# Performance work log

Hardware: AMD Instinct MI355X
Metric: run time of the kernel (lower is better)

Reference implementation:

```python
import jax, jax.numpy as jnp
import numpy as np

NB_KNN = 10
T = 0.07
NUM_CLASSES = 50
EPS = 1e-12  # torch F.normalize eps


def _l2norm(x, axis):
    n = jnp.sqrt(jnp.sum(x * x, axis=axis, keepdims=True))
    return x / jnp.maximum(n, EPS)


def setup_inputs() -> dict:
    key = jax.random.key(0)
    k1, k2, k3 = jax.random.split(key, 3)
    B, N, D = 1024, 200000, 256
    test_features = jax.random.normal(k1, (B, D), dtype=jnp.float32)
    train_features = jax.random.normal(k2, (N, D), dtype=jnp.float32)
    train_labels = jax.random.randint(k3, (N,), 0, NUM_CLASSES, dtype=jnp.int64)
    return {
        "test_features": test_features,
        "train_features": train_features,
        "train_labels": train_labels,
    }


def reference(test_features, train_features, train_labels):
    # Faithful to torch: normalize(train_features.T, dim=1) -> normalize [D, N]
    # along axis 1 (the N axis), exactly as the original module does.
    gallery = _l2norm(train_features.T, axis=1)          # [D, N]
    q = _l2norm(test_features, axis=1)                   # [B, D]
    sim = q @ gallery                                    # [B, N]
    topk_sims, idx = jax.lax.top_k(sim, NB_KNN)          # [B, k], [B, k]
    neighbors_labels = train_labels[idx]                 # [B, k]
    w = jax.nn.softmax(topk_sims / T, axis=1)            # [B, k]
    # one-hot weighted scatter-sum into class scores
    onehot = jax.nn.one_hot(neighbors_labels, NUM_CLASSES, dtype=w.dtype)  # [B, k, C]
    return jnp.sum(onehot * w[:, :, None], axis=1)       # [B, C]
```

## Files before the change

### kernel.cpp

```cpp
#include <hip/hip_runtime.h>
#include <hip/hip_bf16.h>
#include <math.h>
#include <stdint.h>

#define DDIM 256
#define CAP  320
#define NCLS 50

typedef short bf16x8_t __attribute__((ext_vector_type(8)));
typedef float f32x4_t  __attribute__((ext_vector_type(4)));

__device__ __forceinline__ void gl_lds16(const void* g, void* l) {
  __builtin_amdgcn_global_load_lds(
      (__attribute__((address_space(1))) unsigned int*)(uintptr_t)g,
      (__attribute__((address_space(3))) unsigned int*)l,
      16, 0, 0);
}

__global__ void k_cast_colsq(const float* __restrict__ train,
                             __hip_bfloat16* __restrict__ tbf,
                             double* __restrict__ colsq, int N) {
  const int t = threadIdx.x;
  const int nb = gridDim.x;
  const int per = (N + nb - 1) / nb;
  const int r0 = blockIdx.x * per;
  const int r1 = (r0 + per < N) ? (r0 + per) : N;
  double acc = 0.0;
  int r = r0;
  for (; r + 4 <= r1; r += 4) {
    float v0 = train[(size_t)(r + 0) * DDIM + t];
    float v1 = train[(size_t)(r + 1) * DDIM + t];
    float v2 = train[(size_t)(r + 2) * DDIM + t];
    float v3 = train[(size_t)(r + 3) * DDIM + t];
    if (tbf) {
      tbf[(size_t)(r + 0) * DDIM + t] = __float2bfloat16(v0);
      tbf[(size_t)(r + 1) * DDIM + t] = __float2bfloat16(v1);
      tbf[(size_t)(r + 2) * DDIM + t] = __float2bfloat16(v2);
      tbf[(size_t)(r + 3) * DDIM + t] = __float2bfloat16(v3);
    }
    acc = fma((double)v0, (double)v0, acc);
    acc = fma((double)v1, (double)v1, acc);
    acc = fma((double)v2, (double)v2, acc);
    acc = fma((double)v3, (double)v3, acc);
  }
  for (; r < r1; ++r) {
    float v = train[(size_t)r * DDIM + t];
    if (tbf) tbf[(size_t)r * DDIM + t] = __float2bfloat16(v);
    acc = fma((double)v, (double)v, acc);
  }
  atomicAdd(&colsq[t], acc);
}

__global__ void k_prep(const float* __restrict__ test, const double* __restrict__ colsq,
                       float* __restrict__ qs, __hip_bfloat16* __restrict__ qs_bf,
                       float* __restrict__ tau, int B) {
  const int row = blockIdx.x, t = threadIdx.x;
  const int wid = t >> 6, lane = t & 63;
  __shared__ float ps[4];
  __shared__ float stot;
  float v = test[(size_t)row * DDIM + t];
  float ss = v * v;
#pragma unroll
  for (int o = 32; o > 0; o >>= 1) ss += __shfl_down(ss, o, 64);
  if (lane == 0) ps[wid] = ss;
  __syncthreads();
  if (t == 0) stot = ps[0] + ps[1] + ps[2] + ps[3];
  __syncthreads();
  float rn   = fmaxf(sqrtf(stot), 1e-12f);
  float coln = fmaxf(sqrtf((float)colsq[t]), 1e-12f);
  float qv   = (v / rn) / coln;
  qs[(size_t)row * DDIM + t] = qv;
  qs_bf[(size_t)row * DDIM + t] = __float2bfloat16(qv);
  float s2 = qv * qv;
#pragma unroll
  for (int o = 32; o > 0; o >>= 1) s2 += __shfl_down(s2, o, 64);
  if (lane == 0) ps[wid] = s2;
  __syncthreads();
  if (t == 0) tau[row] = 3.30f * sqrtf(ps[0] + ps[1] + ps[2] + ps[3]);
}

__global__ __launch_bounds__(256, 3)
void k_mfma(const __hip_bfloat16* __restrict__ qs_bf,
            const __hip_bfloat16* __restrict__ train_bf,
            const float* __restrict__ tau, int* __restrict__ cidx,
            int* __restrict__ cnt, int N, int B) {
  __shared__ __align__(16) char sAB[2][16384];
  __shared__ float tau_s[128];
  const int tid = threadIdx.x;
  const int w = tid >> 6, lane = tid & 63;
  const int wr = w >> 1, wc = w & 1;
  const int row0 = blockIdx.y * 128;
  const int col0 = blockIdx.x * 128;
  const int l15 = lane & 15, l4 = lane >> 4;

  if (tid < 128) {
    int rr = row0 + tid; if (rr >= B) rr = B - 1;
    tau_s[tid] = tau[rr];
  }

  const int g0 = 2 * w, g1 = 2 * w + 1;
  int ar0 = row0 + g0 * 16 + l15; if (ar0 >= B) ar0 = B - 1;
  int ar1 = row0 + g1 * 16 + l15; if (ar1 >= B) ar1 = B - 1;
  const __hip_bfloat16* aS0 = qs_bf + (size_t)ar0 * DDIM + l4 * 8;
  const __hip_bfloat16* aS1 = qs_bf + (size_t)ar1 * DDIM + l4 * 8;
  int bc0 = col0 + g0 * 16 + l15; if (bc0 >= N) bc0 = N - 1;
  int bc1 = col0 + g1 * 16 + l15; if (bc1 >= N) bc1 = N - 1;
  const __hip_bfloat16* bS0 = train_bf + (size_t)bc0 * DDIM + l4 * 8;
  const __hip_bfloat16* bS1 = train_bf + (size_t)bc1 * DDIM + l4 * 8;

  f32x4_t acc[4][4];
#pragma unroll
  for (int m = 0; m < 4; ++m)
#pragma unroll
    for (int n = 0; n < 4; ++n) acc[m][n] = (f32x4_t){0.f, 0.f, 0.f, 0.f};

  {
    char* A0 = sAB[0]; char* B0 = sAB[0] + 8192;
    gl_lds16(aS0, A0 + g0 * 1024);
    gl_lds16(aS1, A0 + g1 * 1024);
    gl_lds16(bS0, B0 + g0 * 1024);
    gl_lds16(bS1, B0 + g1 * 1024);
  }
  __syncthreads();

  for (int s = 0; s < 8; ++s) {
    const int cur = s & 1;
    if (s < 7) {
      const int ko = (s + 1) * 32;
      char* An = sAB[cur ^ 1]; char* Bn = An + 8192;
      gl_lds16(aS0 + ko, An + g0 * 1024);
      gl_lds16(aS1 + ko, An + g1 * 1024);
      gl_lds16(bS0 + ko, Bn + g0 * 1024);
      gl_lds16(bS1 + ko, Bn + g1 * 1024);
    }
    const char* Ac = sAB[cur]; const char* Bc = Ac + 8192;
    bf16x8_t af[4], bfr[4];
#pragma unroll
    for (int m = 0; m < 4; ++m)
      af[m] = *(const bf16x8_t*)(Ac + (wr * 4 + m) * 1024 + lane * 16);
#pragma unroll
    for (int n = 0; n < 4; ++n)
      bfr[n] = *(const bf16x8_t*)(Bc + (wc * 4 + n) * 1024 + lane * 16);
#pragma unroll
    for (int m = 0; m < 4; ++m)
#pragma unroll
      for (int n = 0; n < 4; ++n)
        acc[m][n] = __builtin_amdgcn_mfma_f32_16x16x32_bf16(af[m], bfr[n],
                                                            acc[m][n], 0, 0, 0);
    __syncthreads();
  }

#pragma unroll
  for (int m = 0; m < 4; ++m) {
#pragma unroll
    for (int n = 0; n < 4; ++n) {
      const int col = col0 + wc * 64 + n * 16 + l15;
      if (col < N) {
#pragma unroll
        for (int r = 0; r < 4; ++r) {
          const int rl = wr * 64 + m * 16 + l4 * 4 + r;
          if (acc[m][n][r] > tau_s[rl] && row0 + rl < B) {
            int p = atomicAdd(&cnt[row0 + rl], 1);
            if (p < CAP) cidx[(size_t)(row0 + rl) * CAP + p] = col;
          }
        }
      }
    }
  }
}

#define DOT4(ACC, A, Bv)                                                     \
  ACC = fmaf((A).x, (Bv).x, ACC); ACC = fmaf((A).y, (Bv).y, ACC);            \
  ACC = fmaf((A).z, (Bv).z, ACC); ACC = fmaf((A).w, (Bv).w, ACC);

__global__ __launch_bounds__(256, 4)
void k_gemm(const float* __restrict__ train, const float* __restrict__ qs,
            const float* __restrict__ tau, int* __restrict__ cidx,
            int* __restrict__ cnt, int N, int B, int tpc) {
  __shared__ float4 As4[8 * 128];
  __shared__ float4 Bs4[8 * 64];
  const int tid = threadIdx.x;
  const int tx = tid & 15, ty = tid >> 4;
  const int wid = tid >> 6, lane = tid & 63;
  const int row0 = blockIdx.y * 128;
  const int colbase = blockIdx.x * tpc * 64;
  float tau_r[8];
#pragma unroll
  for (int i = 0; i < 8; ++i) {
    int r = row0 + ty + 16 * i; if (r >= B) r = B - 1;
    tau_r[i] = tau[r];
  }
  int rL = row0 + lane;      if (rL >= B) rL = B - 1;
  int rH = row0 + 64 + lane; if (rH >= B) rH = B - 1;
  const float* aptrL = qs + (size_t)rL * DDIM;
  const float* aptrH = qs + (size_t)rH * DDIM;
  for (int tile = 0; tile < tpc; ++tile) {
    const int col0 = colbase + tile * 64;
    if (col0 >= N) break;
    int bcol = col0 + lane; if (bcol >= N) bcol = N - 1;
    const float* bptr = train + (size_t)bcol * DDIM;
    float acc[8][4];
#pragma unroll
    for (int i = 0; i < 8; ++i)
#pragma unroll
      for (int j = 0; j < 4; ++j) acc[i][j] = 0.f;
    for (int s = 0; s < 8; ++s) {
      const int kk0 = s * 32;
      __syncthreads();
#pragma unroll
      for (int j = 0; j < 4; ++j) {
        const int slot = wid + 4 * j;
        const int m = slot >> 1, half = slot & 1;
        gl_lds16((half ? aptrH : aptrL) + kk0 + 4 * m, &As4[m * 128 + half * 64]);
      }
#pragma unroll
      for (int j = 0; j < 2; ++j) {
        const int m = wid + 4 * j;
        gl_lds16(bptr + kk0 + 4 * m, &Bs4[m * 64]);
      }
      __syncthreads();
#pragma unroll
      for (int k4 = 0; k4 < 8; ++k4) {
        float4 a[8], b[4];
#pragma unroll
        for (int i = 0; i < 8; ++i) a[i] = As4[k4 * 128 + ty + 16 * i];
#pragma unroll
        for (int j = 0; j < 4; ++j) b[j] = Bs4[k4 * 64 + tx + 16 * j];
#pragma unroll
        for (int i = 0; i < 8; ++i)
#pragma unroll
          for (int j = 0; j < 4; ++j) { DOT4(acc[i][j], a[i], b[j]) }
      }
    }
#pragma unroll
    for (int i = 0; i < 8; ++i) {
      const int r = row0 + ty + 16 * i;
#pragma unroll
      for (int j = 0; j < 4; ++j) {
        const int c = col0 + tx + 16 * j;
        if (acc[i][j] > tau_r[i] && c < N && r < B) {
          int p = atomicAdd(&cnt[r], 1);
          if (p < CAP) cidx[(size_t)r * CAP + p] = c;
        }
      }
    }
  }
}

__global__ void k_fallback(const float* __restrict__ train, const float* __restrict__ qs,
                           int* __restrict__ cidx, int* __restrict__ cnt, int N) {
  const int row = blockIdx.x;
  const int t = threadIdx.x;
  const int c0 = cnt[row];
  if (c0 >= 10 && c0 <= CAP) return;
  __shared__ float q[DDIM];
  if (t < DDIM) q[t] = qs[(size_t)row * DDIM + t];
  __syncthreads();
  float lv[10]; int li[10];
#pragma unroll
  for (int k = 0; k < 10; ++k) { lv[k] = -INFINITY; li[k] = 0x7FFFFFFF; }
  for (int c = t; c < N; c += 256) {
    const float* tr = train + (size_t)c * DDIM;
    float s = 0.f;
    for (int d = 0; d < DDIM; ++d) s = fmaf(q[d], tr[d], s);
    if (s > lv[9]) {
      int p = 9;
      while (p > 0 && s > lv[p - 1]) { lv[p] = lv[p - 1]; li[p] = li[p - 1]; --p; }
      lv[p] = s; li[p] = c;
    }
  }
  __shared__ float rv[256]; __shared__ int ri[256]; __shared__ int rt_[256];
  __shared__ int topi[10];
  int pt = 0;
  for (int k = 0; k < 10; ++k) {
    rv[t] = (pt < 10) ? lv[pt] : -INFINITY;
    ri[t] = (pt < 10) ? li[pt] : 0x7FFFFFFF;
    rt_[t] = t;
    __syncthreads();
    for (int s2 = 128; s2 > 0; s2 >>= 1) {
      if (t < s2) {
        float ov = rv[t + s2]; int oi = ri[t + s2];
        if (ov > rv[t] || (ov == rv[t] && oi < ri[t])) {
          rv[t] = ov; ri[t] = oi; rt_[t] = rt_[t + s2];
        }
      }
      __syncthreads();
    }
    const int win = rt_[0];
    if (t == 0) topi[k] = ri[0];
    __syncthreads();
    if (t == win) ++pt;
  }
  if (t < 10) cidx[(size_t)row * CAP + t] = topi[t];
  if (t == 0) cnt[row] = 10;
}

__global__ void k_rescore(const float* __restrict__ train, const float* __restrict__ qs,
                          const int* __restrict__ cidx, const int* __restrict__ cnt,
                          double* __restrict__ dval) {
  const int row = blockIdx.x;
  const int t = threadIdx.x, wid = t >> 6, lane = t & 63;
  __shared__ float qsh[DDIM];
  if (t < DDIM) qsh[t] = qs[(size_t)row * DDIM + t];
  __syncthreads();
  int n = cnt[row]; if (n > CAP) n = CAP;
  for (int ci = wid; ci < n; ci += 4) {
    const int c = cidx[(size_t)row * CAP + ci];
    const float4 tv = *(const float4*)(train + (size_t)c * DDIM + lane * 4);
    const float4 qv = *(const float4*)(qsh + lane * 4);
    double s = (double)tv.x * qv.x + (double)tv.y * qv.y +
               (double)tv.z * qv.z + (double)tv.w * qv.w;
#pragma unroll
    for (int o = 32; o > 0; o >>= 1) s += __shfl_down(s, o, 64);
    if (lane == 0) dval[(size_t)row * CAP + ci] = s;
  }
}

__global__ void k_finalize(const double* __restrict__ dval, const int* __restrict__ cidx,
                           const int* __restrict__ cnt, const int* __restrict__ labels,
                           float* __restrict__ out) {
  const int row = blockIdx.x;
  const int t = threadIdx.x;
  int n = cnt[row]; if (n > CAP) n = CAP;
  __shared__ double sv[CAP]; __shared__ int si[CAP];
  for (int i = t; i < CAP; i += 256) {
    sv[i] = (i < n) ? dval[(size_t)row * CAP + i] : -INFINITY;
    si[i] = (i < n) ? cidx[(size_t)row * CAP + i] : 0x7FFFFFFF;
  }
  __syncthreads();
  __shared__ double rv[256]; __shared__ int ri[256]; __shared__ int rp[256];
  __shared__ double topv[10]; __shared__ int topl[10];
  __shared__ int wpos;
  for (int k = 0; k < 10; ++k) {
    double bv = sv[t]; int bi = si[t]; int bp = t;
    if (t + 256 < CAP) {
      double v2 = sv[t + 256]; int i2 = si[t + 256];
      if (v2 > bv || (v2 == bv && i2 < bi)) { bv = v2; bi = i2; bp = t + 256; }
    }
    rv[t] = bv; ri[t] = bi; rp[t] = bp;
    __syncthreads();
    for (int s2 = 128; s2 > 0; s2 >>= 1) {
      if (t < s2) {
        double ov = rv[t + s2]; int oi = ri[t + s2];
        if (ov > rv[t] || (ov == rv[t] && oi < ri[t])) {
          rv[t] = ov; ri[t] = oi; rp[t] = rp[t + s2];
        }
      }
      __syncthreads();
    }
    if (t == 0) { topv[k] = rv[0]; topl[k] = ri[0]; wpos = rp[0]; }
    __syncthreads();
    if (t == 0) sv[wpos] = -INFINITY;
    __syncthreads();
  }
  __shared__ double oc[NCLS];
  if (t < NCLS) oc[t] = 0.0;
  __syncthreads();
  if (t == 0) {
    const double m = topv[0];
    double w[10]; double ssum = 0.0;
#pragma unroll
    for (int k = 0; k < 10; ++k) { w[k] = exp((topv[k] - m) / 0.07); ssum += w[k]; }
#pragma unroll
    for (int k = 0; k < 10; ++k) oc[labels[topl[k]]] += w[k] / ssum;
  }
  __syncthreads();
  if (t < NCLS) out[(size_t)row * NCLS + t] = (float)oc[t];
}

extern "C" void kernel_launch(void* const* d_in, const int* in_sizes, int n_in,
                              void* d_out, int out_size, void* d_ws, size_t ws_size,
                              hipStream_t stream) {
  const float* test   = (const float*)d_in[0];
  const float* train  = (const float*)d_in[1];
  const int*   labels = (const int*)d_in[2];
  float* out = (float*)d_out;
  const int B = in_sizes[0] / DDIM;
  const int N = in_sizes[2];
  (void)n_in; (void)out_size;

  char* w = (char*)d_ws;
  size_t off = 0;
  auto alloc = [&](size_t bytes) {
    size_t o = off; off = (off + bytes + 255) & ~(size_t)255; return o;
  };
  double* colsq = (double*)(w + alloc(2048));
  int*    cnt   = (int*)(w + alloc((size_t)B * 4));
  float*  tau   = (float*)(w + alloc((size_t)B * 4));
  float*  qs    = (float*)(w + alloc((size_t)B * DDIM * 4));
  __hip_bfloat16* qs_bf = (__hip_bfloat16*)(w + alloc((size_t)B * DDIM * 2));
  int*    cidx  = (int*)(w + alloc((size_t)B * CAP * 4));
  double* dval  = (double*)(w + alloc((size_t)B * CAP * 8));
  __hip_bfloat16* train_bf = (__hip_bfloat16*)(w + alloc((size_t)N * DDIM * 2));
  const bool use_mfma = (ws_size >= off);

  hipMemsetAsync(d_ws, 0, 2048 + (size_t)B * 4, stream);

  if (use_mfma) {
    hipLaunchKernelGGL(k_cast_colsq, dim3(1024), dim3(256), 0, stream,
                       train, train_bf, colsq, N);
    hipLaunchKernelGGL(k_prep, dim3(B), dim3(256), 0, stream,
                       test, colsq, qs, qs_bf, tau, B);
    hipLaunchKernelGGL(k_mfma, dim3((N + 127) / 128, (B + 127) / 128),
                       dim3(256), 0, stream, qs_bf, train_bf, tau, cidx, cnt, N, B);
  } else {
    hipLaunchKernelGGL(k_cast_colsq, dim3(1024), dim3(256), 0, stream,
                       train, (__hip_bfloat16*)nullptr, colsq, N);
    hipLaunchKernelGGL(k_prep, dim3(B), dim3(256), 0, stream,
                       test, colsq, qs, qs_bf, tau, B);
    const int CT = (N + 63) / 64;
    const int rb = (B + 127) / 128;
    int bx = 2048 / (rb > 0 ? rb : 1); if (bx < 1) bx = 1;
    int tpc = (CT + bx - 1) / bx;
    int chunks = (CT + tpc - 1) / tpc;
    hipLaunchKernelGGL(k_gemm, dim3(chunks, rb), dim3(256), 0, stream,
                       train, qs, tau, cidx, cnt, N, B, tpc);
  }

  hipLaunchKernelGGL(k_fallback, dim3(B), dim3(256), 0, stream,
                     train, qs, cidx, cnt, N);
  hipLaunchKernelGGL(k_rescore,  dim3(B), dim3(256), 0, stream,
                     train, qs, cidx, cnt, dval);
  hipLaunchKernelGGL(k_finalize, dim3(B), dim3(256), 0, stream,
                     dval, cidx, cnt, labels, out);
}
```

Baseline: 619.1 us.

## Keep train tile resident in LDS and stream all query panels per block

The MFMA similarity kernel now loads a full 128-column train tile (all 256 dims, 64KB) into LDS once, then loops over every 128-row query panel. A fragments are read directly from global memory and prefetched one K-step ahead, so the train matrix is read once instead of once per query panel. The cast/column-norm kernel is also vectorized to float4 loads with ushort4 bf16 stores and an LDS reduction, and its grid is halved. The trade-offs are lower occupancy from the 64KB LDS footprint and A operands coming from global/L2 rather than shared memory.

```diff
diff --git a/kernel.cpp b/kernel.cpp
--- a/kernel.cpp
+++ b/kernel.cpp
@@ -17,38 +17,41 @@
       16, 0, 0);
 }
 
+__device__ __forceinline__ unsigned short bf16bits(float v) {
+  __hip_bfloat16 h = __float2bfloat16(v);
+  return *reinterpret_cast<unsigned short*>(&h);
+}
+
 __global__ void k_cast_colsq(const float* __restrict__ train,
                              __hip_bfloat16* __restrict__ tbf,
                              double* __restrict__ colsq, int N) {
   const int t = threadIdx.x;
+  const int rsub = t >> 6;
+  const int c4 = (t & 63) * 4;
   const int nb = gridDim.x;
-  const int per = (N + nb - 1) / nb;
+  int per = (N + nb - 1) / nb; per = (per + 3) & ~3;
   const int r0 = blockIdx.x * per;
-  const int r1 = (r0 + per < N) ? (r0 + per) : N;
-  double acc = 0.0;
-  int r = r0;
-  for (; r + 4 <= r1; r += 4) {
-    float v0 = train[(size_t)(r + 0) * DDIM + t];
-    float v1 = train[(size_t)(r + 1) * DDIM + t];
-    float v2 = train[(size_t)(r + 2) * DDIM + t];
-    float v3 = train[(size_t)(r + 3) * DDIM + t];
+  int r1 = r0 + per; if (r1 > N) r1 = N;
+  double a0 = 0, a1 = 0, a2 = 0, a3 = 0;
+  for (int r = r0 + rsub; r < r1; r += 4) {
+    float4 v = *(const float4*)(train + (size_t)r * DDIM + c4);
     if (tbf) {
-      tbf[(size_t)(r + 0) * DDIM + t] = __float2bfloat16(v0);
-      tbf[(size_t)(r + 1) * DDIM + t] = __float2bfloat16(v1);
-      tbf[(size_t)(r + 2) * DDIM + t] = __float2bfloat16(v2);
-      tbf[(size_t)(r + 3) * DDIM + t] = __float2bfloat16(v3);
-    }
-    acc = fma((double)v0, (double)v0, acc);
-    acc = fma((double)v1, (double)v1, acc);
-    acc = fma((double)v2, (double)v2, acc);
-    acc = fma((double)v3, (double)v3, acc);
-  }
-  for (; r < r1; ++r) {
-    float v = train[(size_t)r * DDIM + t];
-    if (tbf) tbf[(size_t)r * DDIM + t] = __float2bfloat16(v);
-    acc = fma((double)v, (double)v, acc);
-  }
-  atomicAdd(&colsq[t], acc);
+      ushort4 u;
+      u.x = bf16bits(v.x); u.y = bf16bits(v.y);
+      u.z = bf16bits(v.z); u.w = bf16bits(v.w);
+      *(ushort4*)(tbf + (size_t)r * DDIM + c4) = u;
+    }
+    a0 = fma((double)v.x, (double)v.x, a0);
+    a1 = fma((double)v.y, (double)v.y, a1);
+    a2 = fma((double)v.z, (double)v.z, a2);
+    a3 = fma((double)v.w, (double)v.w, a3);
+  }
+  __shared__ double red[4][DDIM];
+  red[rsub][c4 + 0] = a0; red[rsub][c4 + 1] = a1;
+  red[rsub][c4 + 2] = a2; red[rsub][c4 + 3] = a3;
+  __syncthreads();
+  double s = red[0][t] + red[1][t] + red[2][t] + red[3][t];
+  atomicAdd(&colsq[t], s);
 }
 
 __global__ void k_prep(const float* __restrict__ test, const double* __restrict__ colsq,
@@ -79,89 +82,80 @@
   if (t == 0) tau[row] = 3.30f * sqrtf(ps[0] + ps[1] + ps[2] + ps[3]);
 }
 
-__global__ __launch_bounds__(256, 3)
+__global__ __launch_bounds__(256, 2)
 void k_mfma(const __hip_bfloat16* __restrict__ qs_bf,
             const __hip_bfloat16* __restrict__ train_bf,
             const float* __restrict__ tau, int* __restrict__ cidx,
             int* __restrict__ cnt, int N, int B) {
-  __shared__ __align__(16) char sAB[2][16384];
-  __shared__ float tau_s[128];
+  __shared__ __align__(16) char Bsh[65536];
+  __shared__ float tau_s[1024];
   const int tid = threadIdx.x;
   const int w = tid >> 6, lane = tid & 63;
-  const int wr = w >> 1, wc = w & 1;
-  const int row0 = blockIdx.y * 128;
+  const int l15 = lane & 15, l4 = lane >> 4;
   const int col0 = blockIdx.x * 128;
-  const int l15 = lane & 15, l4 = lane >> 4;
-
-  if (tid < 128) {
-    int rr = row0 + tid; if (rr >= B) rr = B - 1;
-    tau_s[tid] = tau[rr];
-  }
-
-  const int g0 = 2 * w, g1 = 2 * w + 1;
-  int ar0 = row0 + g0 * 16 + l15; if (ar0 >= B) ar0 = B - 1;
-  int ar1 = row0 + g1 * 16 + l15; if (ar1 >= B) ar1 = B - 1;
-  const __hip_bfloat16* aS0 = qs_bf + (size_t)ar0 * DDIM + l4 * 8;
-  const __hip_bfloat16* aS1 = qs_bf + (size_t)ar1 * DDIM + l4 * 8;
-  int bc0 = col0 + g0 * 16 + l15; if (bc0 >= N) bc0 = N - 1;
-  int bc1 = col0 + g1 * 16 + l15; if (bc1 >= N) bc1 = N - 1;
-  const __hip_bfloat16* bS0 = train_bf + (size_t)bc0 * DDIM + l4 * 8;
-  const __hip_bfloat16* bS1 = train_bf + (size_t)bc1 * DDIM + l4 * 8;
-
-  f32x4_t acc[4][4];
-#pragma unroll
-  for (int m = 0; m < 4; ++m)
-#pragma unroll
-    for (int n = 0; n < 4; ++n) acc[m][n] = (f32x4_t){0.f, 0.f, 0.f, 0.f};
-
+
+#pragma unroll
+  for (int i = 0; i < 16; ++i) {
+    const int idx = w * 16 + i;
+    const int s = idx >> 3, g = idx & 7;
+    int c = col0 + g * 16 + l15; if (c >= N) c = N - 1;
+    gl_lds16(train_bf + (size_t)c * DDIM + s * 32 + l4 * 8, Bsh + idx * 1024);
+  }
+  for (int i = tid; i < 1024; i += 256) {
+    int rr = i; if (rr >= B) rr = B - 1;
+    tau_s[i] = tau[rr];
+  }
+  __syncthreads();
+
+  const int npan = (B + 127) / 128;
+  bf16x8_t afc[2], afn[2];
   {
-    char* A0 = sAB[0]; char* B0 = sAB[0] + 8192;
-    gl_lds16(aS0, A0 + g0 * 1024);
-    gl_lds16(aS1, A0 + g1 * 1024);
-    gl_lds16(bS0, B0 + g0 * 1024);
-    gl_lds16(bS1, B0 + g1 * 1024);
-  }
-  __syncthreads();
-
-  for (int s = 0; s < 8; ++s) {
-    const int cur = s & 1;
-    if (s < 7) {
-      const int ko = (s + 1) * 32;
-      char* An = sAB[cur ^ 1]; char* Bn = An + 8192;
-      gl_lds16(aS0 + ko, An + g0 * 1024);
-      gl_lds16(aS1 + ko, An + g1 * 1024);
-      gl_lds16(bS0 + ko, Bn + g0 * 1024);
-      gl_lds16(bS1 + ko, Bn + g1 * 1024);
-    }
-    const char* Ac = sAB[cur]; const char* Bc = Ac + 8192;
-    bf16x8_t af[4], bfr[4];
-#pragma unroll
-    for (int m = 0; m < 4; ++m)
-      af[m] = *(const bf16x8_t*)(Ac + (wr * 4 + m) * 1024 + lane * 16);
-#pragma unroll
-    for (int n = 0; n < 4; ++n)
-      bfr[n] = *(const bf16x8_t*)(Bc + (wc * 4 + n) * 1024 + lane * 16);
-#pragma unroll
-    for (int m = 0; m < 4; ++m)
-#pragma unroll
-      for (int n = 0; n < 4; ++n)
-        acc[m][n] = __builtin_amdgcn_mfma_f32_16x16x32_bf16(af[m], bfr[n],
-                                                            acc[m][n], 0, 0, 0);
-    __syncthreads();
-  }
-
-#pragma unroll
-  for (int m = 0; m < 4; ++m) {
-#pragma unroll
-    for (int n = 0; n < 4; ++n) {
-      const int col = col0 + wc * 64 + n * 16 + l15;
-      if (col < N) {
-#pragma unroll
-        for (int r = 0; r < 4; ++r) {
-          const int rl = wr * 64 + m * 16 + l4 * 4 + r;
-          if (acc[m][n][r] > tau_s[rl] && row0 + rl < B) {
-            int p = atomicAdd(&cnt[row0 + rl], 1);
-            if (p < CAP) cidx[(size_t)(row0 + rl) * CAP + p] = col;
+    int r0 = w * 32 + l15;      if (r0 >= B) r0 = B - 1;
+    int r1 = w * 32 + 16 + l15; if (r1 >= B) r1 = B - 1;
+    afc[0] = *(const bf16x8_t*)(qs_bf + (size_t)r0 * DDIM + l4 * 8);
+    afc[1] = *(const bf16x8_t*)(qs_bf + (size_t)r1 * DDIM + l4 * 8);
+  }
+
+  for (int p = 0; p < npan; ++p) {
+    f32x4_t acc[2][8];
+#pragma unroll
+    for (int m = 0; m < 2; ++m)
+#pragma unroll
+      for (int n = 0; n < 8; ++n) acc[m][n] = (f32x4_t){0.f, 0.f, 0.f, 0.f};
+
+#pragma unroll
+    for (int s = 0; s < 8; ++s) {
+      const int sp1 = (s + 1) & 7;
+      const int pn = (s == 7) ? (p + 1 < npan ? p + 1 : p) : p;
+      {
+        int r0 = pn * 128 + w * 32 + l15;      if (r0 >= B) r0 = B - 1;
+        int r1 = pn * 128 + w * 32 + 16 + l15; if (r1 >= B) r1 = B - 1;
+        const size_t ko = (size_t)sp1 * 32 + l4 * 8;
+        afn[0] = *(const bf16x8_t*)(qs_bf + (size_t)r0 * DDIM + ko);
+        afn[1] = *(const bf16x8_t*)(qs_bf + (size_t)r1 * DDIM + ko);
+      }
+#pragma unroll
+      for (int n = 0; n < 8; ++n) {
+        bf16x8_t bf = *(const bf16x8_t*)(Bsh + (s * 8 + n) * 1024 + lane * 16);
+        acc[0][n] = __builtin_amdgcn_mfma_f32_16x16x32_bf16(afc[0], bf, acc[0][n], 0, 0, 0);
+        acc[1][n] = __builtin_amdgcn_mfma_f32_16x16x32_bf16(afc[1], bf, acc[1][n], 0, 0, 0);
+      }
+      afc[0] = afn[0]; afc[1] = afn[1];
+    }
+
+#pragma unroll
+    for (int m = 0; m < 2; ++m) {
+#pragma unroll
+      for (int n = 0; n < 8; ++n) {
+        const int coln = col0 + n * 16 + l15;
+        if (coln < N) {
+#pragma unroll
+          for (int r = 0; r < 4; ++r) {
+            const int rl = p * 128 + w * 32 + m * 16 + l4 * 4 + r;
+            if (rl < B && acc[m][n][r] > tau_s[rl]) {
+              int pos = atomicAdd(&cnt[rl], 1);
+              if (pos < CAP) cidx[(size_t)rl * CAP + pos] = coln;
+            }
           }
         }
       }
@@ -397,14 +391,14 @@
   hipMemsetAsync(d_ws, 0, 2048 + (size_t)B * 4, stream);
 
   if (use_mfma) {
-    hipLaunchKernelGGL(k_cast_colsq, dim3(1024), dim3(256), 0, stream,
+    hipLaunchKernelGGL(k_cast_colsq, dim3(512), dim3(256), 0, stream,
                        train, train_bf, colsq, N);
     hipLaunchKernelGGL(k_prep, dim3(B), dim3(256), 0, stream,
                        test, colsq, qs, qs_bf, tau, B);
-    hipLaunchKernelGGL(k_mfma, dim3((N + 127) / 128, (B + 127) / 128),
-                       dim3(256), 0, stream, qs_bf, train_bf, tau, cidx, cnt, N, B);
+    hipLaunchKernelGGL(k_mfma, dim3((N + 127) / 128), dim3(256), 0, stream,
+                       qs_bf, train_bf, tau, cidx, cnt, N, B);
   } else {
-    hipLaunchKernelGGL(k_cast_colsq, dim3(1024), dim3(256), 0, stream,
+    hipLaunchKernelGGL(k_cast_colsq, dim3(512), dim3(256), 0, stream,
                        train, (__hip_bfloat16*)nullptr, colsq, N);
     hipLaunchKernelGGL(k_prep, dim3(B), dim3(256), 0, stream,
                        test, colsq, qs, qs_bf, tau, B);
```

New measurement: 661.5 us. 6.9% more time.
